# Optimization experiments

Measured on AMD Instinct MI355X. Metric: run time of the kernel, lower is better.

The kernel has to match this reference:

```python
import jax, jax.numpy as jnp
import numpy as np

DIM_IN = 1024
DIM_OUT = 1024
NUM_HEADS = 16
HEAD_DIM = DIM_OUT // NUM_HEADS


def setup_inputs() -> dict:
    key = jax.random.key(0)
    k1, k2, k3, k4 = jax.random.split(key, 4)
    X = jax.random.normal(k1, (4, 2048, DIM_IN), dtype=jnp.float32)
    W_qkv = jax.random.normal(k2, (DIM_IN, 3 * DIM_OUT), dtype=jnp.float32) * (DIM_IN ** -0.5)
    W_out = jax.random.normal(k3, (DIM_OUT, DIM_OUT), dtype=jnp.float32) * (DIM_OUT ** -0.5)
    b_out = jax.random.normal(k4, (DIM_OUT,), dtype=jnp.float32) * 0.01
    return {"X": X, "W_qkv": W_qkv, "W_out": W_out, "b_out": b_out}


def reference(X, W_qkv, W_out, b_out):
    B, S, _ = X.shape
    qkv = X @ W_qkv  # [B, S, 3*dim_out]
    qkv = qkv.reshape(B, S, 3, NUM_HEADS, HEAD_DIM).transpose(2, 0, 3, 1, 4)
    q, k, v = qkv[0], qkv[1], qkv[2]  # each [B, H, S, hd]
    scores = jnp.einsum('bhqd,bhkd->bhqk', q, k)  # [B, H, S, S]
    causal = jnp.triu(jnp.ones((S, S), dtype=bool), k=1)
    scores = jnp.where(causal, -jnp.inf, scores)
    attn = jax.nn.softmax(scores * (HEAD_DIM ** -0.5), axis=-1)
    ctx = jnp.einsum('bhqk,bhkd->bhqd', attn, v)  # [B, H, S, hd]
    ctx = ctx.transpose(0, 2, 1, 3).reshape(B, S, DIM_OUT)
    return ctx @ W_out + b_out
```

## Files before the change

kernel.cpp:

```cpp
#include <hip/hip_runtime.h>
#include <hip/hip_bf16.h>

typedef __bf16 bf16_t;
typedef __bf16 bf16x8 __attribute__((ext_vector_type(8)));
typedef __bf16 bf16x4 __attribute__((ext_vector_type(4)));
typedef float f32x4 __attribute__((ext_vector_type(4)));
typedef float f32x16 __attribute__((ext_vector_type(16)));
typedef unsigned int u32x4 __attribute__((ext_vector_type(4)));

#define AS1(p) ((const __attribute__((address_space(1))) void*)(p))
#define AS3(p) ((__attribute__((address_space(3))) void*)(p))

#define QSCALE 0.1803368801111204f

__global__ void cast_x_kernel(const float* __restrict__ X, bf16_t* __restrict__ Xb) {
  int i = (blockIdx.x * 256 + threadIdx.x) * 4;
  float4 v = *(const float4*)(X + i);
  bf16x4 o;
  o[0] = (bf16_t)v.x; o[1] = (bf16_t)v.y; o[2] = (bf16_t)v.z; o[3] = (bf16_t)v.w;
  *(bf16x4*)(Xb + i) = o;
}

__global__ void transpose_cast_kernel(const float* __restrict__ W, bf16_t* __restrict__ Wt,
                                      int K, int N) {
  __shared__ float tile[32][33];
  int n0 = blockIdx.x * 32, k0 = blockIdx.y * 32;
  int tx = threadIdx.x, ty = threadIdx.y;
  for (int r = ty; r < 32; r += 8)
    tile[r][tx] = W[(size_t)(k0 + r) * N + n0 + tx];
  __syncthreads();
  for (int r = ty; r < 32; r += 8)
    Wt[(size_t)(n0 + r) * K + k0 + tx] = (bf16_t)tile[tx][r];
}

__global__ __launch_bounds__(256) void gemm_qkv_kernel(
    const bf16_t* __restrict__ A, const bf16_t* __restrict__ Bt,
    bf16_t* __restrict__ Qb, bf16_t* __restrict__ Kb, bf16_t* __restrict__ Vt) {
  __shared__ __align__(16) bf16_t As[128 * 32];
  __shared__ __align__(16) bf16_t Bs[128 * 32];
  const int tid = threadIdx.x;
  const int lane = tid & 63, wave = tid >> 6;
  const int quad = lane >> 4, l15 = lane & 15;
  const int wr = wave >> 1, wc = wave & 1;
  const int m0 = blockIdx.x * 128, n0 = blockIdx.y * 128;
  f32x4 acc[4][4];
  const f32x4 vzero = {0.f, 0.f, 0.f, 0.f};
#pragma unroll
  for (int i = 0; i < 4; i++)
#pragma unroll
    for (int j = 0; j < 4; j++) acc[i][j] = vzero;

  for (int kb = 0; kb < 1024; kb += 32) {
    __syncthreads();
#pragma unroll
    for (int i = 0; i < 2; i++) {
      int c = i * 256 + tid;
      int row = c >> 2, kc = c & 3;
      __builtin_amdgcn_global_load_lds(AS1(A + (size_t)(m0 + row) * 1024 + kb + kc * 8),
                                       AS3(As + c * 8), 16, 0, 0);
    }
#pragma unroll
    for (int i = 0; i < 2; i++) {
      int c = i * 256 + tid;
      int row = c >> 2, kc = c & 3;
      __builtin_amdgcn_global_load_lds(AS1(Bt + (size_t)(n0 + row) * 1024 + kb + kc * 8),
                                       AS3(Bs + c * 8), 16, 0, 0);
    }
    __builtin_amdgcn_s_waitcnt(0);
    __syncthreads();
    bf16x8 af[4], bfr[4];
#pragma unroll
    for (int t = 0; t < 4; t++) {
      af[t]  = *(const bf16x8*)(As + (wr * 64 + t * 16 + l15) * 32 + quad * 8);
      bfr[t] = *(const bf16x8*)(Bs + (wc * 64 + t * 16 + l15) * 32 + quad * 8);
    }
#pragma unroll
    for (int mt = 0; mt < 4; mt++)
#pragma unroll
      for (int nt = 0; nt < 4; nt++)
        acc[mt][nt] = __builtin_amdgcn_mfma_f32_16x16x32_bf16(af[mt], bfr[nt], acc[mt][nt], 0, 0, 0);
  }
#pragma unroll
  for (int nt = 0; nt < 4; nt++) {
    int gn = n0 + wc * 64 + nt * 16 + l15;
    int which = gn >> 10;
    int rem = gn & 1023;
    int hh = rem >> 6, dd = rem & 63;
    if (which == 2) {
#pragma unroll
      for (int mt = 0; mt < 4; mt++) {
        int gm0 = m0 + wr * 64 + mt * 16 + quad * 4;
        int b = gm0 >> 11, s = gm0 & 2047;
        bf16x4 o;
#pragma unroll
        for (int r = 0; r < 4; r++) o[r] = (bf16_t)acc[mt][nt][r];
        *(bf16x4*)(Vt + ((size_t)((b << 4) + hh) * 64 + dd) * 2048 + s) = o;
      }
    } else {
      bf16_t* dst = (which == 0) ? Qb : Kb;
      float scl = (which == 0) ? QSCALE : 1.0f;
#pragma unroll
      for (int mt = 0; mt < 4; mt++) {
#pragma unroll
        for (int r = 0; r < 4; r++) {
          int gm = m0 + wr * 64 + mt * 16 + quad * 4 + r;
          int b = gm >> 11, s = gm & 2047;
          dst[((size_t)((b << 4) + hh) * 2048 + s) * 64 + dd] = (bf16_t)(acc[mt][nt][r] * scl);
        }
      }
    }
  }
}

__device__ inline unsigned pack_bf16x2(float a, float b) {
  unsigned short lo = __builtin_bit_cast(unsigned short, (bf16_t)a);
  unsigned short hi = __builtin_bit_cast(unsigned short, (bf16_t)b);
  return (unsigned)lo | ((unsigned)hi << 16);
}

__global__ __launch_bounds__(256, 2) void attn_kernel(
    const bf16_t* __restrict__ Qg_, const bf16_t* __restrict__ Kg_,
    const bf16_t* __restrict__ Vtg_, bf16_t* __restrict__ ctx) {
  __shared__ __align__(16) bf16_t Ksm[2][128 * 64];
  __shared__ __align__(16) bf16_t Vsm[2][64 * 128];
  const int tid = threadIdx.x;
  const int lane = tid & 63, w = tid >> 6;
  const int l31 = lane & 31, hl = lane >> 5;
  const int krow = (l31 & 0x13) | ((l31 & 4) << 1) | ((l31 & 8) >> 1);

  const int bh = blockIdx.x >> 3;
  const int pp = blockIdx.x & 7;
  const int b = bh >> 4, h = bh & 15;
  const size_t base = (size_t)bh * 2048 * 64;
  const bf16_t* Qg = Qg_ + base;
  const bf16_t* Kg = Kg_ + base;
  const bf16_t* Vtg = Vtg_ + base;

  int kadr[4];
#pragma unroll
  for (int kk = 0; kk < 4; kk++)
    kadr[kk] = (krow * 8 + ((kk * 2 + hl) ^ (krow & 7))) * 8;
  int vadr[2];
#pragma unroll
  for (int nv = 0; nv < 2; nv++) {
    const int dr = nv * 32 + l31;
    vadr[nv] = (dr * 16 + (hl ^ (dr & 15))) * 8;
  }

  auto stage_kv = [&](int bb, int jn) {
#pragma unroll
    for (int i = 0; i < 4; i++) {
      int slot = i * 256 + tid;
      int row = slot >> 3, c = (slot & 7) ^ (row & 7);
      __builtin_amdgcn_global_load_lds(AS1(Kg + ((size_t)jn * 128 + row) * 64 + c * 8),
                                       AS3(&Ksm[bb][0] + slot * 8), 16, 0, 0);
    }
#pragma unroll
    for (int i = 0; i < 4; i++) {
      int slot = i * 256 + tid;
      int d = slot >> 4, c = (slot & 15) ^ (d & 15);
      __builtin_amdgcn_global_load_lds(AS1(Vtg + (size_t)d * 2048 + jn * 128 + c * 8),
                                       AS3(&Vsm[bb][0] + slot * 8), 16, 0, 0);
    }
  };

  bf16x8 bone;
#pragma unroll
  for (int e = 0; e < 8; e++) bone[e] = (bf16_t)1.0f;

  int cur = 0;
  stage_kv(0, 0);

  for (int ti = 0; ti < 2; ti++) {
    const int qb = (ti == 0) ? pp : 15 - pp;
    const int L = qb + 1;
    const int qg = qb * 128 + w * 32 + l31;

    bf16x8 aq[4];
#pragma unroll
    for (int kk = 0; kk < 4; kk++)
      aq[kk] = *(const bf16x8*)(Qg + (size_t)qg * 64 + kk * 16 + hl * 8);

    f32x16 Oacc[2], Lacc;
#pragma unroll
    for (int e = 0; e < 16; e++) { Oacc[0][e] = 0.f; Oacc[1][e] = 0.f; Lacc[e] = 0.f; }

    for (int j = 0; j < L; j++) {
      asm volatile("s_waitcnt vmcnt(0)" ::: "memory");
      __syncthreads();
      const bool havenext = (j + 1 < L) || (ti == 0);
      if (havenext) stage_kv(cur ^ 1, (j + 1 < L) ? j + 1 : 0);

      const bf16_t* Kb = &Ksm[cur][0];
      const bf16_t* Vb = &Vsm[cur][0];
      const bool diag = (j == qb);

      auto nt_body = [&](int nt, bool masked) {
        f32x16 sc;
#pragma unroll
        for (int e = 0; e < 16; e++) sc[e] = 0.f;
        __builtin_amdgcn_s_setprio(1);
#pragma unroll
        for (int kk = 0; kk < 4; kk++) {
          bf16x8 ak = *(const bf16x8*)(Kb + nt * 2048 + kadr[kk]);
          sc = __builtin_amdgcn_mfma_f32_32x32x16_bf16(ak, aq[kk], sc, 0, 0, 0);
        }
        __builtin_amdgcn_s_setprio(0);

        float p[16];
#pragma unroll
        for (int r = 0; r < 16; r++) {
          const int koff = hl * 8 + (r & 7) + 16 * (r >> 3);
          float x = sc[r];
          p[r] = (masked && (koff > l31)) ? 0.f : __builtin_exp2f(x);
        }

        u32x4 w0, w1;
        w0[0] = pack_bf16x2(p[0], p[1]);   w0[1] = pack_bf16x2(p[2], p[3]);
        w0[2] = pack_bf16x2(p[4], p[5]);   w0[3] = pack_bf16x2(p[6], p[7]);
        w1[0] = pack_bf16x2(p[8], p[9]);   w1[1] = pack_bf16x2(p[10], p[11]);
        w1[2] = pack_bf16x2(p[12], p[13]); w1[3] = pack_bf16x2(p[14], p[15]);
        bf16x8 pa0 = __builtin_bit_cast(bf16x8, w0);
        bf16x8 pa1 = __builtin_bit_cast(bf16x8, w1);

        __builtin_amdgcn_s_setprio(1);
        Lacc = __builtin_amdgcn_mfma_f32_32x32x16_bf16(pa0, bone, Lacc, 0, 0, 0);
        Lacc = __builtin_amdgcn_mfma_f32_32x32x16_bf16(pa1, bone, Lacc, 0, 0, 0);
#pragma unroll
        for (int nv = 0; nv < 2; nv++) {
          bf16x8 bv0 = *(const bf16x8*)(Vb + (vadr[nv] ^ ((4 * nt) * 8)));
          Oacc[nv] = __builtin_amdgcn_mfma_f32_32x32x16_bf16(pa0, bv0, Oacc[nv], 0, 0, 0);
          bf16x8 bv1 = *(const bf16x8*)(Vb + (vadr[nv] ^ ((4 * nt + 2) * 8)));
          Oacc[nv] = __builtin_amdgcn_mfma_f32_32x32x16_bf16(pa1, bv1, Oacc[nv], 0, 0, 0);
        }
        __builtin_amdgcn_s_setprio(0);
      };

      if (!diag) {
#pragma unroll
        for (int nt = 0; nt < 4; nt++) nt_body(nt, false);
      } else {
#pragma unroll
        for (int nt = 0; nt < 4; nt++)
          if (nt <= w) nt_body(nt, nt == w);
      }
      cur ^= 1;
    }

#pragma unroll
    for (int r = 0; r < 16; r++) {
      const int crow = (r & 3) + 8 * (r >> 2) + 4 * hl;
      const float rl = __builtin_amdgcn_rcpf(Lacc[r]);
      const int qrow = qb * 128 + w * 32 + crow;
#pragma unroll
      for (int nv = 0; nv < 2; nv++)
        ctx[((size_t)b * 2048 + qrow) * 1024 + h * 64 + nv * 32 + l31] =
            (bf16_t)(Oacc[nv][r] * rl);
    }
  }
}

__global__ __launch_bounds__(256) void gemm_out_kernel(
    const bf16_t* __restrict__ A, const bf16_t* __restrict__ Bt,
    const float* __restrict__ bias, float* __restrict__ out) {
  __shared__ __align__(16) bf16_t As[128 * 32];
  __shared__ __align__(16) bf16_t Bs[128 * 32];
  const int tid = threadIdx.x;
  const int lane = tid & 63, wave = tid >> 6;
  const int quad = lane >> 4, l15 = lane & 15;
  const int wr = wave >> 1, wc = wave & 1;
  const int m0 = blockIdx.x * 128, n0 = blockIdx.y * 128;
  f32x4 acc[4][4];
  const f32x4 vzero = {0.f, 0.f, 0.f, 0.f};
#pragma unroll
  for (int i = 0; i < 4; i++)
#pragma unroll
    for (int j = 0; j < 4; j++) acc[i][j] = vzero;

  for (int kb = 0; kb < 1024; kb += 32) {
    __syncthreads();
#pragma unroll
    for (int i = 0; i < 2; i++) {
      int c = i * 256 + tid;
      int row = c >> 2, kc = c & 3;
      __builtin_amdgcn_global_load_lds(AS1(A + (size_t)(m0 + row) * 1024 + kb + kc * 8),
                                       AS3(As + c * 8), 16, 0, 0);
    }
#pragma unroll
    for (int i = 0; i < 2; i++) {
      int c = i * 256 + tid;
      int row = c >> 2, kc = c & 3;
      __builtin_amdgcn_global_load_lds(AS1(Bt + (size_t)(n0 + row) * 1024 + kb + kc * 8),
                                       AS3(Bs + c * 8), 16, 0, 0);
    }
    __builtin_amdgcn_s_waitcnt(0);
    __syncthreads();
    bf16x8 af[4], bfr[4];
#pragma unroll
    for (int t = 0; t < 4; t++) {
      af[t]  = *(const bf16x8*)(As + (wr * 64 + t * 16 + l15) * 32 + quad * 8);
      bfr[t] = *(const bf16x8*)(Bs + (wc * 64 + t * 16 + l15) * 32 + quad * 8);
    }
#pragma unroll
    for (int mt = 0; mt < 4; mt++)
#pragma unroll
      for (int nt = 0; nt < 4; nt++)
        acc[mt][nt] = __builtin_amdgcn_mfma_f32_16x16x32_bf16(af[mt], bfr[nt], acc[mt][nt], 0, 0, 0);
  }
#pragma unroll
  for (int nt = 0; nt < 4; nt++) {
    int gn = n0 + wc * 64 + nt * 16 + l15;
    float bv = bias[gn];
#pragma unroll
    for (int mt = 0; mt < 4; mt++) {
#pragma unroll
      for (int r = 0; r < 4; r++) {
        int gm = m0 + wr * 64 + mt * 16 + quad * 4 + r;
        out[(size_t)gm * 1024 + gn] = acc[mt][nt][r] + bv;
      }
    }
  }
}

extern "C" void kernel_launch(void* const* d_in, const int* in_sizes, int n_in,
                              void* d_out, int out_size, void* d_ws, size_t ws_size,
                              hipStream_t stream) {
  (void)in_sizes; (void)n_in; (void)out_size; (void)ws_size;
  const float* X     = (const float*)d_in[0];
  const float* W_qkv = (const float*)d_in[1];
  const float* W_out = (const float*)d_in[2];
  const float* b_out = (const float*)d_in[3];
  float* out = (float*)d_out;

  char* ws = (char*)d_ws;
  bf16_t* Xb    = (bf16_t*)(ws);
  bf16_t* Wqkvt = (bf16_t*)(ws + 16777216);
  bf16_t* Woutt = (bf16_t*)(ws + 23068672);
  bf16_t* Qb    = (bf16_t*)(ws + 25165824);
  bf16_t* Kb    = (bf16_t*)(ws + 41943040);
  bf16_t* Vt    = (bf16_t*)(ws + 58720256);
  bf16_t* ctx   = (bf16_t*)(ws + 75497472);

  cast_x_kernel<<<8192, 256, 0, stream>>>(X, Xb);
  transpose_cast_kernel<<<dim3(96, 32), dim3(32, 8), 0, stream>>>(W_qkv, Wqkvt, 1024, 3072);
  transpose_cast_kernel<<<dim3(32, 32), dim3(32, 8), 0, stream>>>(W_out, Woutt, 1024, 1024);
  gemm_qkv_kernel<<<dim3(64, 24), 256, 0, stream>>>(Xb, Wqkvt, Qb, Kb, Vt);
  attn_kernel<<<dim3(512), 256, 0, stream>>>(Qb, Kb, Vt, ctx);
  gemm_out_kernel<<<dim3(64, 8), 256, 0, stream>>>(ctx, Woutt, b_out, out);
}
```

Measured before the change: 264.1 us.

## Split attention into one q-block per CTA with 64-key tiles

The attention kernel stops pairing two query blocks per CTA (the balanced pp / 15-pp scheme). It now launches 1024 CTAs, each owning a single 128-row query block, scheduled heaviest first. The K/V tiles shrink from 128 to 64 keys, which halves shared memory, and launch bounds are raised to 4 CTAs per CU so more work is resident. Causal skipping is now per 32-key subtile against each wave's query range. In exchange there are twice as many barrier iterations per key, and the load balance now depends on the hardware scheduler rather than on explicit pairing.

After: 255.2 us. 1.03x faster.

```diff
diff --git a/kernel.cpp b/kernel.cpp
--- a/kernel.cpp
+++ b/kernel.cpp
@@ -118,18 +118,18 @@
   return (unsigned)lo | ((unsigned)hi << 16);
 }
 
-__global__ __launch_bounds__(256, 2) void attn_kernel(
+__global__ __launch_bounds__(256, 4) void attn_kernel(
     const bf16_t* __restrict__ Qg_, const bf16_t* __restrict__ Kg_,
     const bf16_t* __restrict__ Vtg_, bf16_t* __restrict__ ctx) {
-  __shared__ __align__(16) bf16_t Ksm[2][128 * 64];
-  __shared__ __align__(16) bf16_t Vsm[2][64 * 128];
+  __shared__ __align__(16) bf16_t Ksm[2][64 * 64];
+  __shared__ __align__(16) bf16_t Vsm[2][64 * 64];
   const int tid = threadIdx.x;
   const int lane = tid & 63, w = tid >> 6;
   const int l31 = lane & 31, hl = lane >> 5;
   const int krow = (l31 & 0x13) | ((l31 & 4) << 1) | ((l31 & 8) >> 1);
 
-  const int bh = blockIdx.x >> 3;
-  const int pp = blockIdx.x & 7;
+  const int bh = blockIdx.x & 63;
+  const int qb = 15 - (blockIdx.x >> 6);
   const int b = bh >> 4, h = bh & 15;
   const size_t base = (size_t)bh * 2048 * 64;
   const bf16_t* Qg = Qg_ + base;
@@ -144,22 +144,22 @@
 #pragma unroll
   for (int nv = 0; nv < 2; nv++) {
     const int dr = nv * 32 + l31;
-    vadr[nv] = (dr * 16 + (hl ^ (dr & 15))) * 8;
+    vadr[nv] = (dr * 8 + (hl ^ (dr & 7))) * 8;
   }
 
   auto stage_kv = [&](int bb, int jn) {
 #pragma unroll
-    for (int i = 0; i < 4; i++) {
+    for (int i = 0; i < 2; i++) {
       int slot = i * 256 + tid;
       int row = slot >> 3, c = (slot & 7) ^ (row & 7);
-      __builtin_amdgcn_global_load_lds(AS1(Kg + ((size_t)jn * 128 + row) * 64 + c * 8),
+      __builtin_amdgcn_global_load_lds(AS1(Kg + ((size_t)jn * 64 + row) * 64 + c * 8),
                                        AS3(&Ksm[bb][0] + slot * 8), 16, 0, 0);
     }
 #pragma unroll
-    for (int i = 0; i < 4; i++) {
+    for (int i = 0; i < 2; i++) {
       int slot = i * 256 + tid;
-      int d = slot >> 4, c = (slot & 15) ^ (d & 15);
-      __builtin_amdgcn_global_load_lds(AS1(Vtg + (size_t)d * 2048 + jn * 128 + c * 8),
+      int d = slot >> 3, c = (slot & 7) ^ (d & 7);
+      __builtin_amdgcn_global_load_lds(AS1(Vtg + (size_t)d * 2048 + jn * 64 + c * 8),
                                        AS3(&Vsm[bb][0] + slot * 8), 16, 0, 0);
     }
   };
@@ -167,96 +167,91 @@
   bf16x8 bone;
 #pragma unroll
   for (int e = 0; e < 8; e++) bone[e] = (bf16_t)1.0f;
+  f32x16 zc;
+#pragma unroll
+  for (int e = 0; e < 16; e++) zc[e] = 0.f;
+
+  const int J = 2 * (qb + 1);
+  const int qrel = qb * 128 + w * 32;
+  const int qg = qrel + l31;
+
+  bf16x8 aq[4];
+#pragma unroll
+  for (int kk = 0; kk < 4; kk++)
+    aq[kk] = *(const bf16x8*)(Qg + (size_t)qg * 64 + kk * 16 + hl * 8);
+
+  f32x16 Oacc[2], Lacc;
+#pragma unroll
+  for (int e = 0; e < 16; e++) { Oacc[0][e] = 0.f; Oacc[1][e] = 0.f; Lacc[e] = 0.f; }
 
   int cur = 0;
   stage_kv(0, 0);
 
-  for (int ti = 0; ti < 2; ti++) {
-    const int qb = (ti == 0) ? pp : 15 - pp;
-    const int L = qb + 1;
-    const int qg = qb * 128 + w * 32 + l31;
-
-    bf16x8 aq[4];
-#pragma unroll
-    for (int kk = 0; kk < 4; kk++)
-      aq[kk] = *(const bf16x8*)(Qg + (size_t)qg * 64 + kk * 16 + hl * 8);
-
-    f32x16 Oacc[2], Lacc;
-#pragma unroll
-    for (int e = 0; e < 16; e++) { Oacc[0][e] = 0.f; Oacc[1][e] = 0.f; Lacc[e] = 0.f; }
-
-    for (int j = 0; j < L; j++) {
-      asm volatile("s_waitcnt vmcnt(0)" ::: "memory");
-      __syncthreads();
-      const bool havenext = (j + 1 < L) || (ti == 0);
-      if (havenext) stage_kv(cur ^ 1, (j + 1 < L) ? j + 1 : 0);
-
-      const bf16_t* Kb = &Ksm[cur][0];
-      const bf16_t* Vb = &Vsm[cur][0];
-      const bool diag = (j == qb);
-
-      auto nt_body = [&](int nt, bool masked) {
-        f32x16 sc;
-#pragma unroll
-        for (int e = 0; e < 16; e++) sc[e] = 0.f;
-        __builtin_amdgcn_s_setprio(1);
-#pragma unroll
-        for (int kk = 0; kk < 4; kk++) {
-          bf16x8 ak = *(const bf16x8*)(Kb + nt * 2048 + kadr[kk]);
-          sc = __builtin_amdgcn_mfma_f32_32x32x16_bf16(ak, aq[kk], sc, 0, 0, 0);
-        }
-        __builtin_amdgcn_s_setprio(0);
-
-        float p[16];
-#pragma unroll
-        for (int r = 0; r < 16; r++) {
-          const int koff = hl * 8 + (r & 7) + 16 * (r >> 3);
-          float x = sc[r];
-          p[r] = (masked && (koff > l31)) ? 0.f : __builtin_exp2f(x);
-        }
-
-        u32x4 w0, w1;
-        w0[0] = pack_bf16x2(p[0], p[1]);   w0[1] = pack_bf16x2(p[2], p[3]);
-        w0[2] = pack_bf16x2(p[4], p[5]);   w0[3] = pack_bf16x2(p[6], p[7]);
-        w1[0] = pack_bf16x2(p[8], p[9]);   w1[1] = pack_bf16x2(p[10], p[11]);
-        w1[2] = pack_bf16x2(p[12], p[13]); w1[3] = pack_bf16x2(p[14], p[15]);
-        bf16x8 pa0 = __builtin_bit_cast(bf16x8, w0);
-        bf16x8 pa1 = __builtin_bit_cast(bf16x8, w1);
-
-        __builtin_amdgcn_s_setprio(1);
-        Lacc = __builtin_amdgcn_mfma_f32_32x32x16_bf16(pa0, bone, Lacc, 0, 0, 0);
-        Lacc = __builtin_amdgcn_mfma_f32_32x32x16_bf16(pa1, bone, Lacc, 0, 0, 0);
-#pragma unroll
-        for (int nv = 0; nv < 2; nv++) {
-          bf16x8 bv0 = *(const bf16x8*)(Vb + (vadr[nv] ^ ((4 * nt) * 8)));
-          Oacc[nv] = __builtin_amdgcn_mfma_f32_32x32x16_bf16(pa0, bv0, Oacc[nv], 0, 0, 0);
-          bf16x8 bv1 = *(const bf16x8*)(Vb + (vadr[nv] ^ ((4 * nt + 2) * 8)));
-          Oacc[nv] = __builtin_amdgcn_mfma_f32_32x32x16_bf16(pa1, bv1, Oacc[nv], 0, 0, 0);
-        }
-        __builtin_amdgcn_s_setprio(0);
-      };
-
-      if (!diag) {
-#pragma unroll
-        for (int nt = 0; nt < 4; nt++) nt_body(nt, false);
-      } else {
-#pragma unroll
-        for (int nt = 0; nt < 4; nt++)
-          if (nt <= w) nt_body(nt, nt == w);
-      }
-      cur ^= 1;
-    }
-
-#pragma unroll
-    for (int r = 0; r < 16; r++) {
-      const int crow = (r & 3) + 8 * (r >> 2) + 4 * hl;
-      const float rl = __builtin_amdgcn_rcpf(Lacc[r]);
-      const int qrow = qb * 128 + w * 32 + crow;
-#pragma unroll
-      for (int nv = 0; nv < 2; nv++)
-        ctx[((size_t)b * 2048 + qrow) * 1024 + h * 64 + nv * 32 + l31] =
-            (bf16_t)(Oacc[nv][r] * rl);
-    }
+  for (int j = 0; j < J; j++) {
+    asm volatile("s_waitcnt vmcnt(0)" ::: "memory");
+    __syncthreads();
+    if (j + 1 < J) stage_kv(cur ^ 1, j + 1);
+
+    const bf16_t* Kb = &Ksm[cur][0];
+    const bf16_t* Vb = &Vsm[cur][0];
+    const int k0 = j * 64;
+
+    auto nt_body = [&](int nt, bool masked) {
+      __builtin_amdgcn_s_setprio(1);
+      bf16x8 ak = *(const bf16x8*)(Kb + nt * 2048 + kadr[0]);
+      f32x16 sc = __builtin_amdgcn_mfma_f32_32x32x16_bf16(ak, aq[0], zc, 0, 0, 0);
+#pragma unroll
+      for (int kk = 1; kk < 4; kk++) {
+        ak = *(const bf16x8*)(Kb + nt * 2048 + kadr[kk]);
+        sc = __builtin_amdgcn_mfma_f32_32x32x16_bf16(ak, aq[kk], sc, 0, 0, 0);
+      }
+      __builtin_amdgcn_s_setprio(0);
+
+      float p[16];
+#pragma unroll
+      for (int r = 0; r < 16; r++) {
+        const int koff = hl * 8 + (r & 7) + 16 * (r >> 3);
+        p[r] = (masked && (koff > l31)) ? 0.f : __builtin_exp2f(sc[r]);
+      }
+
+      u32x4 w0, w1;
+      w0[0] = pack_bf16x2(p[0], p[1]);   w0[1] = pack_bf16x2(p[2], p[3]);
+      w0[2] = pack_bf16x2(p[4], p[5]);   w0[3] = pack_bf16x2(p[6], p[7]);
+      w1[0] = pack_bf16x2(p[8], p[9]);   w1[1] = pack_bf16x2(p[10], p[11]);
+      w1[2] = pack_bf16x2(p[12], p[13]); w1[3] = pack_bf16x2(p[14], p[15]);
+      bf16x8 pa0 = __builtin_bit_cast(bf16x8, w0);
+      bf16x8 pa1 = __builtin_bit_cast(bf16x8, w1);
+
+      __builtin_amdgcn_s_setprio(1);
+      Lacc = __builtin_amdgcn_mfma_f32_32x32x16_bf16(pa0, bone, Lacc, 0, 0, 0);
+      Lacc = __builtin_amdgcn_mfma_f32_32x32x16_bf16(pa1, bone, Lacc, 0, 0, 0);
+#pragma unroll
+      for (int nv = 0; nv < 2; nv++) {
+        bf16x8 bv0 = *(const bf16x8*)(Vb + (vadr[nv] ^ ((nt * 4 + 0) * 8)));
+        Oacc[nv] = __builtin_amdgcn_mfma_f32_32x32x16_bf16(pa0, bv0, Oacc[nv], 0, 0, 0);
+        bf16x8 bv1 = *(const bf16x8*)(Vb + (vadr[nv] ^ ((nt * 4 + 2) * 8)));
+        Oacc[nv] = __builtin_amdgcn_mfma_f32_32x32x16_bf16(pa1, bv1, Oacc[nv], 0, 0, 0);
+      }
+      __builtin_amdgcn_s_setprio(0);
+    };
+
+#pragma unroll
+    for (int nt = 0; nt < 2; nt++) {
+      const int kk0 = k0 + nt * 32;
+      if (kk0 <= qrel) nt_body(nt, kk0 == qrel);
+    }
+    cur ^= 1;
+  }
+
+#pragma unroll
+  for (int r = 0; r < 16; r++) {
+    const int crow = (r & 3) + 8 * (r >> 2) + 4 * hl;
+    const float rl = __builtin_amdgcn_rcpf(Lacc[r]);
+    const int qrow = qb * 128 + w * 32 + crow;
+#pragma unroll
+    for (int nv = 0; nv < 2; nv++)
+      ctx[((size_t)b * 2048 + qrow) * 1024 + h * 64 + nv * 32 + l31] =
+          (bf16_t)(Oacc[nv][r] * rl);
   }
 }
 
@@ -345,6 +340,6 @@
   transpose_cast_kernel<<<dim3(96, 32), dim3(32, 8), 0, stream>>>(W_qkv, Wqkvt, 1024, 3072);
   transpose_cast_kernel<<<dim3(32, 32), dim3(32, 8), 0, stream>>>(W_out, Woutt, 1024, 1024);
   gemm_qkv_kernel<<<dim3(64, 24), 256, 0, stream>>>(Xb, Wqkvt, Qb, Kb, Vt);
-  attn_kernel<<<dim3(512), 256, 0, stream>>>(Qb, Kb, Vt, ctx);
+  attn_kernel<<<dim3(1024), 256, 0, stream>>>(Qb, Kb, Vt, ctx);
   gemm_out_kernel<<<dim3(64, 8), 256, 0, stream>>>(ctx, Woutt, b_out, out);
 }
```
